# Optimization experiments

Measured on AMD Instinct MI355X. Metric: run time of the kernel, lower is better.

The kernel has to match this reference:

```python
import jax, jax.numpy as jnp
import numpy as np

THR = 0.2
TEMPERATURE = 0.1


def setup_inputs() -> dict:
    key = jax.random.key(0)
    k0, k1 = jax.random.split(key)
    N, L, S, C = 4, 4096, 4096, 256
    feat_c0 = jax.random.normal(k0, (N, L, C), dtype=jnp.float32)
    feat_c1 = jax.random.normal(k1, (N, S, C), dtype=jnp.float32)
    return {"feat_c0": feat_c0, "feat_c1": feat_c1}


def reference(feat_c0, feat_c1):
    C = feat_c0.shape[-1]
    scale = 1.0 / (float(C) ** 0.5)
    f0 = feat_c0 * scale  # [N, L, C]
    f1 = feat_c1 * scale  # [N, S, C]

    # sim_matrix = -cdist(f0, f1) / temperature / C  (Euclidean distance)
    sq0 = jnp.sum(f0 * f0, axis=-1)  # [N, L]
    sq1 = jnp.sum(f1 * f1, axis=-1)  # [N, S]
    inner = jnp.einsum('nlc,nsc->nls', f0, f1)  # [N, L, S]
    d2 = jnp.maximum(sq0[:, :, None] + sq1[:, None, :] - 2.0 * inner, 0.0)
    dist = jnp.sqrt(d2)
    sim_matrix = -dist / (TEMPERATURE * C)

    # dual softmax
    conf_matrix0 = jax.nn.softmax(sim_matrix, axis=1)
    conf_matrix1 = jax.nn.softmax(sim_matrix, axis=2)
    conf_matrix = conf_matrix0 * conf_matrix1

    # mutual-nearest-neighbor + threshold matching (dense, jit-friendly form)
    mask = conf_matrix > THR
    i_mask = conf_matrix == jnp.max(conf_matrix, axis=2, keepdims=True)
    j_mask = conf_matrix == jnp.max(conf_matrix, axis=1, keepdims=True)
    mask = mask & i_mask & j_mask  # [N, L, S]

    mask_v = jnp.any(mask, axis=2)                  # [N, L] — row i has a match
    all_j_ids = jnp.argmax(mask, axis=2)            # [N, L] — matched column j
    mconf = jnp.take_along_axis(conf_matrix, all_j_ids[:, :, None], axis=2)[:, :, 0]
    mconf = jnp.where(mask_v, mconf, 0.0)           # [N, L] dense match confidence

    return (conf_matrix, conf_matrix0, conf_matrix1, sim_matrix,
            mask_v, all_j_ids, mconf)
```

## Files before the change

### kernel.cpp

```cpp
#include <hip/hip_runtime.h>
#include <stdint.h>

#define NB 4
#define LD 4096
#define SD 4096
#define CD 256

static constexpr long CHUNK = (long)NB * LD * SD;
static constexpr float SCALE = 0.0625f;
static constexpr float INV_TC = 1.0f / 25.6f;
static constexpr float THRV = 0.2f;

typedef __attribute__((ext_vector_type(8))) short bf16x8;
typedef __attribute__((ext_vector_type(4))) float f32x4;

__device__ __forceinline__ unsigned short f2bf(float x) {
  unsigned int u = __float_as_uint(x);
  return (unsigned short)((u + 0x7FFFu + ((u >> 16) & 1u)) >> 16);
}

__device__ __forceinline__ void gload_lds16(const void* g, void* l) {
  __builtin_amdgcn_global_load_lds((const __attribute__((address_space(1))) void*)g,
                                   (__attribute__((address_space(3))) void*)l, 16, 0, 0);
}

__global__ __launch_bounds__(256) void k_prep(const float* __restrict__ f0,
                                              const float* __restrict__ f1,
                                              unsigned short* __restrict__ abf,
                                              unsigned short* __restrict__ bbf,
                                              float* __restrict__ sq0,
                                              float* __restrict__ sq1) {
  int wid = threadIdx.x >> 6, lane = threadIdx.x & 63;
  long row = (long)blockIdx.x * 4 + wid;
  const long nl = (long)NB * LD;
  const float* src;
  unsigned short* dst;
  float* sqd;
  if (row < nl) {
    src = f0 + row * CD; dst = abf + row * CD; sqd = sq0 + row;
  } else {
    long r = row - nl;
    src = f1 + r * CD; dst = bbf + r * CD; sqd = sq1 + r;
  }
  float4 v = reinterpret_cast<const float4*>(src)[lane];
  v.x *= SCALE; v.y *= SCALE; v.z *= SCALE; v.w *= SCALE;
  ushort4 o;
  o.x = f2bf(v.x); o.y = f2bf(v.y); o.z = f2bf(v.z); o.w = f2bf(v.w);
  reinterpret_cast<ushort4*>(dst)[lane] = o;
  float s = v.x * v.x + v.y * v.y + v.z * v.z + v.w * v.w;
  #pragma unroll
  for (int m = 1; m < 64; m <<= 1) s += __shfl_xor(s, m);
  if (lane == 0) *sqd = s;
}

__global__ __launch_bounds__(256) void k_gemm(const unsigned short* __restrict__ abf,
                                              const unsigned short* __restrict__ bbf,
                                              const float* __restrict__ sq0,
                                              const float* __restrict__ sq1,
                                              float* __restrict__ simout,
                                              float* __restrict__ rowsum,
                                              float* __restrict__ colsum) {
  __shared__ char lds[32768];
  int t = threadIdx.x;
  int wid = t >> 6, lane = t & 63;
  int bz = blockIdx.z;
  long tileM = (long)blockIdx.y * 128;
  long tileS = (long)blockIdx.x * 128;
  const char* aB = (const char*)(abf + ((long)bz * LD + tileM) * CD);
  const char* bB = (const char*)(bbf + ((long)bz * SD + tileS) * CD);

  int srow = t >> 3;
  int scolb = (t & 7) << 4;
  int wrb = (wid >> 1) << 6;
  int wcb = (wid & 1) << 6;
  int lrow = lane & 15;
  int kgrp = lane >> 4;

  f32x4 acc[4][4];
  #pragma unroll
  for (int m = 0; m < 4; ++m)
    #pragma unroll
    for (int n = 0; n < 4; ++n)
      acc[m][n] = (f32x4){0.f, 0.f, 0.f, 0.f};

  for (int kt = 0; kt < 4; ++kt) {
    #pragma unroll
    for (int i = 0; i < 4; ++i) {
      int row = i * 32 + srow;
      int sc = scolb ^ ((row & 7) << 4);
      gload_lds16(aB + (long)row * (CD * 2) + kt * 128 + sc,
                  lds + i * 4096 + (wid << 10));
      gload_lds16(bB + (long)row * (CD * 2) + kt * 128 + sc,
                  lds + 16384 + i * 4096 + (wid << 10));
    }
    __syncthreads();
    #pragma unroll
    for (int ks = 0; ks < 2; ++ks) {
      int kb = ks * 64 + kgrp * 16;
      bf16x8 af[4], bfr[4];
      #pragma unroll
      for (int m = 0; m < 4; ++m) {
        int r = wrb + m * 16 + lrow;
        af[m] = *(const bf16x8*)(lds + r * 128 + (kb ^ ((r & 7) << 4)));
      }
      #pragma unroll
      for (int n = 0; n < 4; ++n) {
        int r = wcb + n * 16 + lrow;
        bfr[n] = *(const bf16x8*)(lds + 16384 + r * 128 + (kb ^ ((r & 7) << 4)));
      }
      #pragma unroll
      for (int m = 0; m < 4; ++m)
        #pragma unroll
        for (int n = 0; n < 4; ++n)
          acc[m][n] = __builtin_amdgcn_mfma_f32_16x16x32_bf16(af[m], bfr[n], acc[m][n], 0, 0, 0);
    }
    __syncthreads();
  }

  long gcol0 = (long)bz * SD + tileS + wcb;
  float sq1v[4];
  #pragma unroll
  for (int n = 0; n < 4; ++n) sq1v[n] = sq1[gcol0 + n * 16 + lrow];

  float ce[4] = {0.f, 0.f, 0.f, 0.f};
  #pragma unroll
  for (int m = 0; m < 4; ++m) {
    #pragma unroll
    for (int i = 0; i < 4; ++i) {
      int lr = m * 16 + kgrp * 4 + i;
      long gl = tileM + wrb + lr;
      float s0 = sq0[(long)bz * LD + gl];
      float* srow_p = simout + ((long)bz * LD + gl) * SD + tileS + wcb;
      float rs = 0.f;
      #pragma unroll
      for (int n = 0; n < 4; ++n) {
        float inner = acc[m][n][i];
        float d2 = fmaxf(s0 + sq1v[n] - 2.0f * inner, 0.f);
        float sv = -__builtin_sqrtf(d2) * INV_TC;
        srow_p[n * 16 + lrow] = sv;
        float e = __expf(sv);
        rs += e;
        ce[n] += e;
      }
      #pragma unroll
      for (int d = 1; d < 16; d <<= 1) rs += __shfl_xor(rs, d);
      if (lrow == 0) atomicAdd(&rowsum[(long)bz * LD + gl], rs);
    }
  }
  #pragma unroll
  for (int n = 0; n < 4; ++n) {
    float cs = ce[n];
    cs += __shfl_xor(cs, 16);
    cs += __shfl_xor(cs, 32);
    if (kgrp == 0) atomicAdd(&colsum[gcol0 + n * 16 + lrow], cs);
  }
}

__global__ __launch_bounds__(256) void k_softmax(const float* __restrict__ sim,
                                                 const float* __restrict__ rowsum,
                                                 const float* __restrict__ colsum,
                                                 float* __restrict__ conf,
                                                 float* __restrict__ conf0,
                                                 float* __restrict__ conf1,
                                                 unsigned long long* __restrict__ rowpack,
                                                 unsigned long long* __restrict__ colpack) {
  __shared__ unsigned long long rmx[64];
  __shared__ unsigned long long cmx[512];
  int t = threadIdx.x;
  if (t < 64) rmx[t] = 0ull;
  cmx[t] = 0ull;
  cmx[t + 256] = 0ull;
  __syncthreads();

  int n = blockIdx.z;
  long rbase = (long)blockIdx.y * 64;
  long cbase = (long)blockIdx.x * 512;
  int c4 = t & 127;
  int rpar = t >> 7;
  long col0 = cbase + (long)c4 * 4;

  f32x4 csv = *(const f32x4*)(colsum + (long)n * SD + col0);
  f32x4 invc;
  invc[0] = 1.0f / csv[0]; invc[1] = 1.0f / csv[1];
  invc[2] = 1.0f / csv[2]; invc[3] = 1.0f / csv[3];

  unsigned long long cpk[4] = {0ull, 0ull, 0ull, 0ull};

  for (int j = 0; j < 32; ++j) {
    int r = rpar + j * 2;
    long gr = rbase + r;
    float invr = 1.0f / rowsum[(long)n * LD + gr];
    long idx = ((long)n * LD + gr) * SD + col0;
    f32x4 sv = *(const f32x4*)(sim + idx);
    f32x4 cf, c0v, c1v;
    unsigned long long best = 0ull;
    #pragma unroll
    for (int q = 0; q < 4; ++q) {
      float e = __expf(sv[q]);
      float a0 = e * invc[q];
      float a1 = e * invr;
      float c = a0 * a1;
      c0v[q] = a0; c1v[q] = a1; cf[q] = c;
      unsigned long long pk = ((unsigned long long)__float_as_uint(c) << 32) |
                              (unsigned int)(~(unsigned int)(col0 + q));
      best = pk > best ? pk : best;
      cpk[q] = pk > cpk[q] ? pk : cpk[q];
    }
    *(f32x4*)(conf + idx) = cf;
    *(f32x4*)(conf0 + idx) = c0v;
    *(f32x4*)(conf1 + idx) = c1v;
    #pragma unroll
    for (int d = 1; d < 64; d <<= 1) {
      unsigned long long o = __shfl_xor(best, d);
      best = o > best ? o : best;
    }
    if ((t & 63) == 0) atomicMax(&rmx[r], best);
  }
  #pragma unroll
  for (int q = 0; q < 4; ++q) atomicMax(&cmx[c4 * 4 + q], cpk[q]);
  __syncthreads();
  if (t < 64) atomicMax(&rowpack[(long)n * LD + rbase + t], rmx[t]);
  atomicMax(&colpack[(long)n * SD + cbase + t], cmx[t]);
  atomicMax(&colpack[(long)n * SD + cbase + 256 + t], cmx[t + 256]);
}

__global__ __launch_bounds__(256) void k_final(const unsigned long long* __restrict__ rowpack,
                                               const unsigned long long* __restrict__ colpack,
                                               float* __restrict__ maskv,
                                               float* __restrict__ jids,
                                               float* __restrict__ mconf) {
  long idx = (long)blockIdx.x * 256 + threadIdx.x;
  if (idx >= (long)NB * LD) return;
  int n = (int)(idx / LD);
  unsigned long long rp = rowpack[idx];
  unsigned int cbits = (unsigned int)(rp >> 32);
  float cval = __uint_as_float(cbits);
  unsigned int col = ~(unsigned int)rp;
  bool valid = (cval > THRV) && (col < (unsigned int)SD);
  if (valid) {
    unsigned long long cp = colpack[(long)n * SD + col];
    valid = ((unsigned int)(cp >> 32)) == cbits;
  }
  maskv[idx] = valid ? 1.0f : 0.0f;
  jids[idx]  = valid ? (float)col : 0.0f;
  mconf[idx] = valid ? cval : 0.0f;
}

extern "C" void kernel_launch(void* const* d_in, const int* in_sizes, int n_in,
                              void* d_out, int out_size, void* d_ws, size_t ws_size,
                              hipStream_t stream) {
  const float* f0 = (const float*)d_in[0];
  const float* f1 = (const float*)d_in[1];
  float* out = (float*)d_out;
  float* conf  = out;
  float* conf0 = out + CHUNK;
  float* conf1 = out + 2 * CHUNK;
  float* simo  = out + 3 * CHUNK;
  float* maskv = out + 4 * CHUNK;
  float* jids  = maskv + (long)NB * LD;
  float* mconf = jids + (long)NB * LD;

  char* ws = (char*)d_ws;
  float* rowsum = (float*)ws;
  float* colsum = (float*)(ws + 65536);
  unsigned long long* rowpack = (unsigned long long*)(ws + 131072);
  unsigned long long* colpack = (unsigned long long*)(ws + 262144);
  hipMemsetAsync(d_ws, 0, 393216, stream);

  unsigned short* abf = (unsigned short*)conf;
  unsigned short* bbf = (unsigned short*)((char*)conf + 8388608);
  float* sq0 = (float*)((char*)conf + 16777216);
  float* sq1 = (float*)((char*)conf + 16777216 + 65536);

  k_prep<<<dim3((NB * (LD + SD)) / 4), dim3(256), 0, stream>>>(f0, f1, abf, bbf, sq0, sq1);
  k_gemm<<<dim3(SD / 128, LD / 128, NB), dim3(256), 0, stream>>>(abf, bbf, sq0, sq1,
                                                                 simo, rowsum, colsum);
  k_softmax<<<dim3(SD / 512, LD / 64, NB), dim3(256), 0, stream>>>(simo, rowsum, colsum,
                                                                   conf, conf0, conf1,
                                                                   rowpack, colpack);
  k_final<<<dim3((NB * LD + 255) / 256), dim3(256), 0, stream>>>(rowpack, colpack,
                                                                 maskv, jids, mconf);
}
```

Before: 385.6 us.

## Recompute GEMM in second pass to fuse softmax outputs and skip sim round-trip

```diff
diff --git a/kernel.cpp b/kernel.cpp
--- a/kernel.cpp
+++ b/kernel.cpp
@@ -53,22 +53,9 @@
   if (lane == 0) *sqd = s;
 }
 
-__global__ __launch_bounds__(256) void k_gemm(const unsigned short* __restrict__ abf,
-                                              const unsigned short* __restrict__ bbf,
-                                              const float* __restrict__ sq0,
-                                              const float* __restrict__ sq1,
-                                              float* __restrict__ simout,
-                                              float* __restrict__ rowsum,
-                                              float* __restrict__ colsum) {
-  __shared__ char lds[32768];
-  int t = threadIdx.x;
+__device__ __forceinline__ void gemm_core(const char* aB, const char* bB, char* lds,
+                                          int t, f32x4 (&acc)[4][4]) {
   int wid = t >> 6, lane = t & 63;
-  int bz = blockIdx.z;
-  long tileM = (long)blockIdx.y * 128;
-  long tileS = (long)blockIdx.x * 128;
-  const char* aB = (const char*)(abf + ((long)bz * LD + tileM) * CD);
-  const char* bB = (const char*)(bbf + ((long)bz * SD + tileS) * CD);
-
   int srow = t >> 3;
   int scolb = (t & 7) << 4;
   int wrb = (wid >> 1) << 6;
@@ -76,7 +63,6 @@
   int lrow = lane & 15;
   int kgrp = lane >> 4;
 
-  f32x4 acc[4][4];
   #pragma unroll
   for (int m = 0; m < 4; ++m)
     #pragma unroll
@@ -116,6 +102,27 @@
     }
     __syncthreads();
   }
+}
+
+__global__ __launch_bounds__(256) void k_pass1(const unsigned short* __restrict__ abf,
+                                               const unsigned short* __restrict__ bbf,
+                                               const float* __restrict__ sq0,
+                                               const float* __restrict__ sq1,
+                                               float* __restrict__ rowsum,
+                                               float* __restrict__ colsum) {
+  __shared__ char lds[32768];
+  int t = threadIdx.x;
+  int wid = t >> 6, lane = t & 63;
+  int wrb = (wid >> 1) << 6, wcb = (wid & 1) << 6;
+  int lrow = lane & 15, kgrp = lane >> 4;
+  int bz = blockIdx.z;
+  long tileM = (long)blockIdx.y * 128;
+  long tileS = (long)blockIdx.x * 128;
+  const char* aB = (const char*)(abf + ((long)bz * LD + tileM) * CD);
+  const char* bB = (const char*)(bbf + ((long)bz * SD + tileS) * CD);
+
+  f32x4 acc[4][4];
+  gemm_core(aB, bB, lds, t, acc);
 
   long gcol0 = (long)bz * SD + tileS + wcb;
   float sq1v[4];
@@ -130,14 +137,12 @@
       int lr = m * 16 + kgrp * 4 + i;
       long gl = tileM + wrb + lr;
       float s0 = sq0[(long)bz * LD + gl];
-      float* srow_p = simout + ((long)bz * LD + gl) * SD + tileS + wcb;
       float rs = 0.f;
       #pragma unroll
       for (int n = 0; n < 4; ++n) {
         float inner = acc[m][n][i];
         float d2 = fmaxf(s0 + sq1v[n] - 2.0f * inner, 0.f);
         float sv = -__builtin_sqrtf(d2) * INV_TC;
-        srow_p[n * 16 + lrow] = sv;
         float e = __expf(sv);
         rs += e;
         ce[n] += e;
@@ -156,72 +161,86 @@
   }
 }
 
-__global__ __launch_bounds__(256) void k_softmax(const float* __restrict__ sim,
-                                                 const float* __restrict__ rowsum,
-                                                 const float* __restrict__ colsum,
-                                                 float* __restrict__ conf,
-                                                 float* __restrict__ conf0,
-                                                 float* __restrict__ conf1,
-                                                 unsigned long long* __restrict__ rowpack,
-                                                 unsigned long long* __restrict__ colpack) {
-  __shared__ unsigned long long rmx[64];
-  __shared__ unsigned long long cmx[512];
+__global__ __launch_bounds__(256) void k_pass2(const unsigned short* __restrict__ abf,
+                                               const unsigned short* __restrict__ bbf,
+                                               const float* __restrict__ sq0,
+                                               const float* __restrict__ sq1,
+                                               const float* __restrict__ rowsum,
+                                               const float* __restrict__ colsum,
+                                               float* __restrict__ simo,
+                                               float* __restrict__ conf,
+                                               float* __restrict__ conf0,
+                                               float* __restrict__ conf1,
+                                               unsigned long long* __restrict__ rowpack,
+                                               unsigned long long* __restrict__ colpack) {
+  __shared__ char lds[32768];
   int t = threadIdx.x;
-  if (t < 64) rmx[t] = 0ull;
-  cmx[t] = 0ull;
-  cmx[t + 256] = 0ull;
-  __syncthreads();
-
-  int n = blockIdx.z;
-  long rbase = (long)blockIdx.y * 64;
-  long cbase = (long)blockIdx.x * 512;
-  int c4 = t & 127;
-  int rpar = t >> 7;
-  long col0 = cbase + (long)c4 * 4;
-
-  f32x4 csv = *(const f32x4*)(colsum + (long)n * SD + col0);
-  f32x4 invc;
-  invc[0] = 1.0f / csv[0]; invc[1] = 1.0f / csv[1];
-  invc[2] = 1.0f / csv[2]; invc[3] = 1.0f / csv[3];
-
+  int wid = t >> 6, lane = t & 63;
+  int wrb = (wid >> 1) << 6, wcb = (wid & 1) << 6;
+  int lrow = lane & 15, kgrp = lane >> 4;
+  int bz = blockIdx.z;
+  long tileM = (long)blockIdx.y * 128;
+  long tileS = (long)blockIdx.x * 128;
+  const char* aB = (const char*)(abf + ((long)bz * LD + tileM) * CD);
+  const char* bB = (const char*)(bbf + ((long)bz * SD + tileS) * CD);
+
+  f32x4 acc[4][4];
+  gemm_core(aB, bB, lds, t, acc);
+
+  long gcol0 = (long)bz * SD + tileS + wcb;
+  float sq1v[4], invc[4];
   unsigned long long cpk[4] = {0ull, 0ull, 0ull, 0ull};
-
-  for (int j = 0; j < 32; ++j) {
-    int r = rpar + j * 2;
-    long gr = rbase + r;
-    float invr = 1.0f / rowsum[(long)n * LD + gr];
-    long idx = ((long)n * LD + gr) * SD + col0;
-    f32x4 sv = *(const f32x4*)(sim + idx);
-    f32x4 cf, c0v, c1v;
-    unsigned long long best = 0ull;
-    #pragma unroll
-    for (int q = 0; q < 4; ++q) {
-      float e = __expf(sv[q]);
-      float a0 = e * invc[q];
-      float a1 = e * invr;
-      float c = a0 * a1;
-      c0v[q] = a0; c1v[q] = a1; cf[q] = c;
-      unsigned long long pk = ((unsigned long long)__float_as_uint(c) << 32) |
-                              (unsigned int)(~(unsigned int)(col0 + q));
-      best = pk > best ? pk : best;
-      cpk[q] = pk > cpk[q] ? pk : cpk[q];
+  #pragma unroll
+  for (int n = 0; n < 4; ++n) {
+    sq1v[n] = sq1[gcol0 + n * 16 + lrow];
+    invc[n] = 1.0f / colsum[gcol0 + n * 16 + lrow];
+  }
+
+  #pragma unroll
+  for (int m = 0; m < 4; ++m) {
+    #pragma unroll
+    for (int i = 0; i < 4; ++i) {
+      int lr = m * 16 + kgrp * 4 + i;
+      long grow = (long)bz * LD + tileM + wrb + lr;
+      float s0 = sq0[grow];
+      float invr = 1.0f / rowsum[grow];
+      long obase = grow * SD + tileS + wcb;
+      unsigned long long rbest = 0ull;
+      #pragma unroll
+      for (int n = 0; n < 4; ++n) {
+        float inner = acc[m][n][i];
+        float d2 = fmaxf(s0 + sq1v[n] - 2.0f * inner, 0.f);
+        float sv = -__builtin_sqrtf(d2) * INV_TC;
+        float e = __expf(sv);
+        float a0 = e * invc[n];
+        float a1 = e * invr;
+        float c = a0 * a1;
+        long oi = obase + n * 16 + lrow;
+        simo[oi] = sv;
+        conf0[oi] = a0;
+        conf1[oi] = a1;
+        conf[oi] = c;
+        unsigned int colg = (unsigned int)(tileS + wcb + n * 16 + lrow);
+        unsigned long long pk = ((unsigned long long)__float_as_uint(c) << 32) |
+                                (unsigned int)(~colg);
+        rbest = pk > rbest ? pk : rbest;
+        cpk[n] = pk > cpk[n] ? pk : cpk[n];
+      }
+      #pragma unroll
+      for (int d = 1; d < 16; d <<= 1) {
+        unsigned long long o = __shfl_xor(rbest, d);
+        rbest = o > rbest ? o : rbest;
+      }
+      if (lrow == 0) atomicMax(&rowpack[grow], rbest);
     }
-    *(f32x4*)(conf + idx) = cf;
-    *(f32x4*)(conf0 + idx) = c0v;
-    *(f32x4*)(conf1 + idx) = c1v;
-    #pragma unroll
-    for (int d = 1; d < 64; d <<= 1) {
-      unsigned long long o = __shfl_xor(best, d);
-      best = o > best ? o : best;
-    }
-    if ((t & 63) == 0) atomicMax(&rmx[r], best);
-  }
-  #pragma unroll
-  for (int q = 0; q < 4; ++q) atomicMax(&cmx[c4 * 4 + q], cpk[q]);
-  __syncthreads();
-  if (t < 64) atomicMax(&rowpack[(long)n * LD + rbase + t], rmx[t]);
-  atomicMax(&colpack[(long)n * SD + cbase + t], cmx[t]);
-  atomicMax(&colpack[(long)n * SD + cbase + 256 + t], cmx[t + 256]);
+  }
+  #pragma unroll
+  for (int n = 0; n < 4; ++n) {
+    unsigned long long b = cpk[n];
+    unsigned long long o = __shfl_xor(b, 16); b = o > b ? o : b;
+    o = __shfl_xor(b, 32); b = o > b ? o : b;
+    if (kgrp == 0) atomicMax(&colpack[gcol0 + n * 16 + lrow], b);
+  }
 }
 
 __global__ __launch_bounds__(256) void k_final(const unsigned long long* __restrict__ rowpack,
@@ -261,23 +280,24 @@
   float* mconf = jids + (long)NB * LD;
 
   char* ws = (char*)d_ws;
-  float* rowsum = (float*)ws;
-  float* colsum = (float*)(ws + 65536);
-  unsigned long long* rowpack = (unsigned long long*)(ws + 131072);
-  unsigned long long* colpack = (unsigned long long*)(ws + 262144);
-  hipMemsetAsync(d_ws, 0, 393216, stream);
-
-  unsigned short* abf = (unsigned short*)conf;
-  unsigned short* bbf = (unsigned short*)((char*)conf + 8388608);
-  float* sq0 = (float*)((char*)conf + 16777216);
-  float* sq1 = (float*)((char*)conf + 16777216 + 65536);
+  unsigned short* abf = (unsigned short*)ws;
+  unsigned short* bbf = (unsigned short*)(ws + 8388608);
+  float* sq0 = (float*)(ws + 16777216);
+  float* sq1 = (float*)(ws + 16777216 + 65536);
+  char* accums = ws + 16908288;
+  float* rowsum = (float*)accums;
+  float* colsum = (float*)(accums + 65536);
+  unsigned long long* rowpack = (unsigned long long*)(accums + 131072);
+  unsigned long long* colpack = (unsigned long long*)(accums + 262144);
+  hipMemsetAsync(accums, 0, 393216, stream);
 
   k_prep<<<dim3((NB * (LD + SD)) / 4), dim3(256), 0, stream>>>(f0, f1, abf, bbf, sq0, sq1);
-  k_gemm<<<dim3(SD / 128, LD / 128, NB), dim3(256), 0, stream>>>(abf, bbf, sq0, sq1,
-                                                                 simo, rowsum, colsum);
-  k_softmax<<<dim3(SD / 512, LD / 64, NB), dim3(256), 0, stream>>>(simo, rowsum, colsum,
-                                                                   conf, conf0, conf1,
-                                                                   rowpack, colpack);
+  k_pass1<<<dim3(SD / 128, LD / 128, NB), dim3(256), 0, stream>>>(abf, bbf, sq0, sq1,
+                                                                  rowsum, colsum);
+  k_pass2<<<dim3(SD / 128, LD / 128, NB), dim3(256), 0, stream>>>(abf, bbf, sq0, sq1,
+                                                                  rowsum, colsum,
+                                                                  simo, conf, conf0, conf1,
+                                                                  rowpack, colpack);
   k_final<<<dim3((NB * LD + 255) / 256), dim3(256), 0, stream>>>(rowpack, colpack,
                                                                  maskv, jids, mconf);
 }
```

Measured after the change: 526.8 us. 36.6% more time.
